# Optimization experiments

Measured on AMD Instinct MI355X. Metric: run time of the kernel, lower is better.

## Reference

```python
import jax, jax.numpy as jnp
import numpy as np
from jax import lax

CH = 16      # channel_n
HID = 128    # hidden_n
WDIM = 128   # w_dim


def _sobel_weight():
    sx = np.array([[-1, 0, 1], [-2, 0, 2], [-1, 0, 1]], dtype=np.float32).reshape(1, 1, 3, 3)
    sy = np.array([[-1, -2, -1], [0, 0, 0], [1, 2, 1]], dtype=np.float32).reshape(1, 1, 3, 3)
    sx = np.repeat(sx, CH, axis=0)  # [16,1,3,3]
    sy = np.repeat(sy, CH, axis=0)  # [16,1,3,3]
    return jnp.asarray(np.concatenate([sx, sy], axis=0))  # [32,1,3,3] torch grouped-conv OIHW layout


def setup_inputs() -> dict:
    key = jax.random.key(0)
    k1, k2, k3, k4 = jax.random.split(key, 4)
    B, H, W = 8, 96, 96
    x = jax.random.uniform(k1, (B, CH, H, W), dtype=jnp.float32)
    w = jax.random.normal(k2, (B, WDIM), dtype=jnp.float32)
    sobel = _sobel_weight()
    # update_net params. NOTE: original fills W2 with 0.0 (trivial delta); we use
    W1 = jax.random.normal(k3, (HID, 3 * CH + WDIM), dtype=jnp.float32) * 0.05
    b1 = jnp.zeros((HID,), dtype=jnp.float32)
    W2 = jax.random.normal(k4, (CH, HID), dtype=jnp.float32) * 0.02
    return {"x": x, "w": w, "sobel": sobel, "W1": W1, "b1": b1, "W2": W2, "steps": 64}


def _living_mask(alpha):
    # max_pool2d(3, stride=1, pad=1) > 0.1 ; torch pads with -inf for max pool
    m = lax.reduce_window(alpha, -jnp.inf, lax.max, (1, 1, 3, 3), (1, 1, 1, 1), 'SAME')
    return m > 0.1


def reference(x, w, sobel, W1, b1, W2, steps):
    B, _, H, Wd = x.shape
    w_exp = jnp.broadcast_to(w[:, :, None, None], (B, WDIM, H, Wd))

    def step(xc, key):
        pre_life = _living_mask(xc[:, 3:4])
        perception = lax.conv_general_dilated(
            xc, sobel, (1, 1), 'SAME', feature_group_count=CH,
            dimension_numbers=('NCHW', 'OIHW', 'NCHW'))  # [B,32,H,W]
        comb = jnp.concatenate([xc, perception, w_exp], axis=1)  # [B,176,H,W]
        h = jax.nn.relu(jnp.einsum('bchw,nc->bnhw', comb, W1) + b1[None, :, None, None])
        delta = jnp.einsum('bnhw,cn->bchw', h, W2)
        alpha = xc[:, 3:4]
        upd = (jax.random.uniform(key, alpha.shape) < 0.5) & (alpha > 0.1)
        xn = xc + delta * upd.astype(xc.dtype)
        life = pre_life & _living_mask(xn[:, 3:4])
        xn = xn * life.astype(xn.dtype)
        return xn, None

    keys = jax.random.split(jax.random.key(42), steps)
    x_final, _ = lax.scan(step, x, keys)
    return x_final
```

## Files before the change

### kernel.cpp

```cpp
#include <hip/hip_runtime.h>
#include <stdint.h>


#define CHN 16
#define HIDN 128
#define WD 128
#define NB 8
#define NH 96
#define NW 96
#define NSTEPS 64
#define TW 16
#define TH 4
#define PLANE (NH*NW)
#define TILES_X (NW/TW)
#define TILES_Y (NH/TH)
#define TPI (TILES_X*TILES_Y)
#define NBLK (NB*TPI)
#define HW_ (TH+2)
#define WW_ (TW+2)
#define NF4 (HW_*WW_*4)
#define NT 256

typedef float v2f __attribute__((ext_vector_type(2)));

__host__ __device__ __forceinline__ uint32_t rotl(uint32_t v, int d){ return (v<<d)|(v>>(32-d)); }

__host__ __device__ __forceinline__ void threefry2x32(uint32_t k0, uint32_t k1,
                                                      uint32_t x0, uint32_t x1,
                                                      uint32_t &o0, uint32_t &o1){
  uint32_t k2 = k0 ^ k1 ^ 0x1BD11BDAu;
  x0 += k0; x1 += k1;
  x0 += x1; x1 = rotl(x1,13); x1 ^= x0;
  x0 += x1; x1 = rotl(x1,15); x1 ^= x0;
  x0 += x1; x1 = rotl(x1,26); x1 ^= x0;
  x0 += x1; x1 = rotl(x1, 6); x1 ^= x0;
  x0 += k1; x1 += k2 + 1u;
  x0 += x1; x1 = rotl(x1,17); x1 ^= x0;
  x0 += x1; x1 = rotl(x1,29); x1 ^= x0;
  x0 += x1; x1 = rotl(x1,16); x1 ^= x0;
  x0 += x1; x1 = rotl(x1,24); x1 ^= x0;
  x0 += k2; x1 += k0 + 2u;
  x0 += x1; x1 = rotl(x1,13); x1 ^= x0;
  x0 += x1; x1 = rotl(x1,15); x1 ^= x0;
  x0 += x1; x1 = rotl(x1,26); x1 ^= x0;
  x0 += x1; x1 = rotl(x1, 6); x1 ^= x0;
  x0 += k0; x1 += k1 + 3u;
  x0 += x1; x1 = rotl(x1,17); x1 ^= x0;
  x0 += x1; x1 = rotl(x1,29); x1 ^= x0;
  x0 += x1; x1 = rotl(x1,16); x1 ^= x0;
  x0 += x1; x1 = rotl(x1,24); x1 ^= x0;
  x0 += k1; x1 += k2 + 4u;
  x0 += x1; x1 = rotl(x1,13); x1 ^= x0;
  x0 += x1; x1 = rotl(x1,15); x1 ^= x0;
  x0 += x1; x1 = rotl(x1,26); x1 ^= x0;
  x0 += x1; x1 = rotl(x1, 6); x1 ^= x0;
  x0 += k2; x1 += k0 + 5u;
  o0 = x0; o1 = x1;
}

__global__ __launch_bounds__(256) void nca_pre(
    const float* __restrict__ w, const float* __restrict__ W1,
    const float* __restrict__ b1, const float* __restrict__ W2,
    float* __restrict__ w1eff, float* __restrict__ w2t, float* __restrict__ c1)
{
  const int b = blockIdx.x, t = threadIdx.x;
  if (b == 0){
    for (int idx = t; idx < HIDN*32; idx += 256){
      int n = idx >> 5, k = idx & 31;
      float v;
      if (k < 16) v = W1[n*176 + k];
      else { int cc = k - 16; v = W1[n*176 + 16 + 2*cc] + W1[n*176 + 17 + 2*cc]; }
      w1eff[idx] = v;
    }
    for (int idx = t; idx < HIDN*CHN; idx += 256){
      int n = idx >> 4, cc = idx & 15;
      w2t[idx] = W2[cc*HIDN + n];
    }
  }
  if (t < HIDN){
    float s = b1[t];
    const float* wrow = W1 + t*176 + 48;
    const float* wb = w + b*WD;
    #pragma unroll 8
    for (int k = 0; k < WD; ++k) s = fmaf(wrow[k], wb[k], s);
    c1[b*HIDN + t] = s;
  }
}

template<bool FIRST>
__global__ __launch_bounds__(NT, 4) void nca_step(
    const float* __restrict__ Xin,
    const unsigned char* __restrict__ Mp,
    const float* __restrict__ w1eff, const float* __restrict__ w2t,
    const float* __restrict__ c1,
    uint32_t key0, uint32_t key1,
    float* __restrict__ Yn, unsigned char* __restrict__ Mn)
{
  __shared__ __align__(16) float w1s[64*32];
  __shared__ __align__(16) float xs[HW_][WW_][20];
  __shared__ float ya[TH+4][TW+4];
  __shared__ float lifes[HW_][WW_];
  __shared__ float ufs[64];

  float* red2p = &xs[0][0][0];
  #define RED2(bk,ch,p) red2p[((((bk)<<4)+(ch))<<6)+(p)]

  const int T = blockIdx.x;
  const int b = T & 7;
  const int t = T >> 3;
  const int tw0 = (t % TILES_X)*TW, th0 = (t / TILES_X)*TH;
  const int tid = threadIdx.x;

  {
    const float4* src = (const float4*)(w1eff + 64*32);
    float4* dst = (float4*)w1s;
    #pragma unroll
    for (int i = 0; i < 2; ++i) dst[tid + i*NT] = src[tid + i*NT];
  }

  if (FIRST){
    for (int idx = tid; idx < CHN*HW_*WW_; idx += NT){
      int ch = idx / (HW_*WW_), rem = idx % (HW_*WW_);
      int hh = rem / WW_, ww = rem % WW_;
      int g2 = th0 - 1 + hh, w2 = tw0 - 1 + ww;
      float v = 0.f;
      if ((unsigned)g2 < NH && (unsigned)w2 < NW)
        v = Xin[((b*CHN + ch)*NH + g2)*NW + w2];
      xs[hh][ww][ch] = v;
    }
  } else {
    if (tid < (TH+4)*(TW+4)){
      int hh = tid / (TW+4), ww = tid % (TW+4);
      int g2 = th0 - 2 + hh, w2 = tw0 - 2 + ww;
      float v = 0.f;
      if ((unsigned)g2 < NH && (unsigned)w2 < NW)
        v = Xin[(size_t)(b*PLANE + g2*NW + w2)*CHN + 3];
      ya[hh][ww] = v;
    }
    float4 xr[2];
    #pragma unroll
    for (int i = 0; i < 2; ++i){
      int idx = tid + i*NT;
      float4 v = make_float4(0.f,0.f,0.f,0.f);
      if (idx < NF4){
        int hh = idx / (WW_*4);
        int rem = idx % (WW_*4);
        int ww = rem >> 2, k4 = rem & 3;
        int g2 = th0 - 1 + hh, w2 = tw0 - 1 + ww;
        if ((unsigned)g2 < NH && (unsigned)w2 < NW)
          v = *(const float4*)(Xin + (size_t)(b*PLANE + g2*NW + w2)*CHN + k4*4);
      }
      xr[i] = v;
    }
    __syncthreads();
    if (tid < HW_*WW_){
      int hh = tid / WW_, ww = tid % WW_;
      int g2 = th0 - 1 + hh, w2 = tw0 - 1 + ww;
      float lf = 0.f;
      if ((unsigned)g2 < NH && (unsigned)w2 < NW){
        float mx = ya[hh][ww];
        #pragma unroll
        for (int dr = 0; dr < 3; ++dr)
          #pragma unroll
          for (int dc = 0; dc < 3; ++dc)
            mx = fmaxf(mx, ya[hh+dr][ww+dc]);
        lf = (Mp[b*PLANE + g2*NW + w2] && (mx > 0.1f)) ? 1.f : 0.f;
      }
      lifes[hh][ww] = lf;
    }
    __syncthreads();
    #pragma unroll
    for (int i = 0; i < 2; ++i){
      int idx = tid + i*NT;
      if (idx < NF4){
        int hh = idx / (WW_*4);
        int rem = idx % (WW_*4);
        int ww = rem >> 2, k4 = rem & 3;
        float lf = lifes[hh][ww];
        float4 v = xr[i];
        v.x *= lf; v.y *= lf; v.z *= lf; v.w *= lf;
        *(float4*)&xs[hh][ww][k4*4] = v;
      }
    }
  }
  __syncthreads();

  const int px = tid & 63;
  const int q  = tid >> 6;
  const int c = px & 15, r = px >> 4;
  const int gh = th0 + r, gw = tw0 + c;
  const int pos = b*PLANE + gh*NW + gw;

  #define LD4(dr,dc,k4) (*(const float4*)&xs[r+(dr)][c+(dc)][(k4)*4])
  const v2f two = (v2f){2.f, 2.f};
  float4 xc4[4];
  v2f xp[8], pp[8];
  #pragma unroll
  for (int k4 = 0; k4 < 4; ++k4){
    xc4[k4] = LD4(1,1,k4);
    xp[2*k4]   = (v2f){xc4[k4].x, xc4[k4].y};
    xp[2*k4+1] = (v2f){xc4[k4].z, xc4[k4].w};
  }
  #pragma unroll
  for (int k4 = 0; k4 < 2; ++k4){
    float4 a = LD4(0,2,k4), b0 = LD4(0,0,k4);
    float4 d = LD4(1,2,k4), e = LD4(1,0,k4);
    float4 f = LD4(2,2,k4), g = LD4(2,0,k4);
    v2f a0 = (v2f){a.x,a.y}, a1 = (v2f){a.z,a.w};
    v2f b0v= (v2f){b0.x,b0.y},b1v= (v2f){b0.z,b0.w};
    v2f d0 = (v2f){d.x,d.y}, d1 = (v2f){d.z,d.w};
    v2f e0 = (v2f){e.x,e.y}, e1 = (v2f){e.z,e.w};
    v2f f0 = (v2f){f.x,f.y}, f1 = (v2f){f.z,f.w};
    v2f g0 = (v2f){g.x,g.y}, g1 = (v2f){g.z,g.w};
    pp[2*k4]   = (a0-b0v) + two*(d0-e0) + (f0-g0);
    pp[2*k4+1] = (a1-b1v) + two*(d1-e1) + (f1-g1);
  }
  #pragma unroll
  for (int k4 = 2; k4 < 4; ++k4){
    float4 a = LD4(2,0,k4), b0 = LD4(0,0,k4);
    float4 d = LD4(2,1,k4), e = LD4(0,1,k4);
    float4 f = LD4(2,2,k4), g = LD4(0,2,k4);
    v2f a0 = (v2f){a.x,a.y}, a1 = (v2f){a.z,a.w};
    v2f b0v= (v2f){b0.x,b0.y},b1v= (v2f){b0.z,b0.w};
    v2f d0 = (v2f){d.x,d.y}, d1 = (v2f){d.z,d.w};
    v2f e0 = (v2f){e.x,e.y}, e1 = (v2f){e.z,e.w};
    v2f f0 = (v2f){f.x,f.y}, f1 = (v2f){f.z,f.w};
    v2f g0 = (v2f){g.x,g.y}, g1 = (v2f){g.z,g.w};
    pp[2*k4]   = (a0-b0v) + two*(d0-e0) + (f0-g0);
    pp[2*k4+1] = (a1-b1v) + two*(d1-e1) + (f1-g1);
  }
  #undef LD4

  if (q == 0){
    uint32_t o0, o1;
    threefry2x32(key0, key1, 0u, (uint32_t)pos, o0, o1);
    ufs[px] = ((((o0 ^ o1) >> 31) == 0u) && (xc4[0].w > 0.1f)) ? 1.f : 0.f;
  } else if (q == 1){
    float mx = xs[r][c][3];
    #pragma unroll
    for (int dr = 0; dr < 3; ++dr)
      #pragma unroll
      for (int dc = 0; dc < 3; ++dc)
        mx = fmaxf(mx, xs[r+dr][c+dc][3]);
    Mn[pos] = (mx > 0.1f) ? (unsigned char)1 : (unsigned char)0;
  }

  const int qq = __builtin_amdgcn_readfirstlane(q);
  float4 myx = xc4[0];
  if (qq == 1) myx = xc4[1];
  else if (qq == 2) myx = xc4[2];
  else if (qq == 3) myx = xc4[3];

  v2f acc2[8];
  #pragma unroll
  for (int i = 0; i < 8; ++i) acc2[i] = (v2f){0.f, 0.f};
  const int nbase = qq << 5;
  const float* c1b = c1 + b*HIDN;

  if (qq < 2){
    #pragma unroll 2
    for (int nn = 0; nn < 32; ++nn){
      const int n = nbase + nn;
      const v2f* wx = (const v2f*)(w1eff + (n << 5));
      v2f h01 = (v2f){c1b[n], 0.f};
      v2f h23 = (v2f){0.f, 0.f};
      #pragma unroll
      for (int k = 0; k < 8; ++k){
        h01 = __builtin_elementwise_fma(xp[k], wx[k],   h01);
        h23 = __builtin_elementwise_fma(pp[k], wx[8+k], h23);
      }
      float hv = fmaxf((h01.x + h01.y) + (h23.x + h23.y), 0.f);
      v2f hvv = (v2f){hv, hv};
      const v2f* w2p = (const v2f*)(w2t + (n << 4));
      #pragma unroll
      for (int cc2 = 0; cc2 < 8; ++cc2)
        acc2[cc2] = __builtin_elementwise_fma(hvv, w2p[cc2], acc2[cc2]);
    }
  } else {
    #pragma unroll 2
    for (int nn = 0; nn < 32; ++nn){
      const int n = nbase + nn;
      const v2f* wx = (const v2f*)(w1s + ((n - 64) << 5));
      v2f h01 = (v2f){c1b[n], 0.f};
      v2f h23 = (v2f){0.f, 0.f};
      #pragma unroll
      for (int k = 0; k < 8; ++k){
        h01 = __builtin_elementwise_fma(xp[k], wx[k],   h01);
        h23 = __builtin_elementwise_fma(pp[k], wx[8+k], h23);
      }
      float hv = fmaxf((h01.x + h01.y) + (h23.x + h23.y), 0.f);
      v2f hvv = (v2f){hv, hv};
      const v2f* w2p = (const v2f*)(w2t + (n << 4));
      #pragma unroll
      for (int cc2 = 0; cc2 < 8; ++cc2)
        acc2[cc2] = __builtin_elementwise_fma(hvv, w2p[cc2], acc2[cc2]);
    }
  }

  __syncthreads();

  if (q >= 2){
    #pragma unroll
    for (int cc2 = 0; cc2 < 8; ++cc2){
      RED2(q-2, 2*cc2  , px) = acc2[cc2].x;
      RED2(q-2, 2*cc2+1, px) = acc2[cc2].y;
    }
  }
  __syncthreads();
  if (q < 2){
    #pragma unroll
    for (int cc2 = 0; cc2 < 8; ++cc2){
      acc2[cc2].x += RED2(q, 2*cc2  , px);
      acc2[cc2].y += RED2(q, 2*cc2+1, px);
    }
    #pragma unroll
    for (int cc2 = 0; cc2 < 8; ++cc2){
      RED2(q, 2*cc2  , px) = acc2[cc2].x;
      RED2(q, 2*cc2+1, px) = acc2[cc2].y;
    }
  }
  __syncthreads();

  {
    float uf = ufs[px];
    int ch = q << 2;
    float v0 = RED2(0, ch+0, px) + RED2(1, ch+0, px);
    float v1 = RED2(0, ch+1, px) + RED2(1, ch+1, px);
    float v2 = RED2(0, ch+2, px) + RED2(1, ch+2, px);
    float v3 = RED2(0, ch+3, px) + RED2(1, ch+3, px);
    float4 o = make_float4(fmaf(v0, uf, myx.x), fmaf(v1, uf, myx.y),
                           fmaf(v2, uf, myx.z), fmaf(v3, uf, myx.w));
    *(float4*)(Yn + (size_t)pos*CHN + q*4) = o;
  }
  #undef RED2
}

__global__ __launch_bounds__(256) void nca_final(
    const float* __restrict__ Yp, const unsigned char* __restrict__ Mp,
    float* __restrict__ out)
{
  __shared__ float ya[TH+4][TW+4];
  __shared__ float lifes[TH][TW];
  const int T = blockIdx.x;
  const int b = T & 7;
  const int t = T >> 3;
  const int tw0 = (t % TILES_X)*TW, th0 = (t / TILES_X)*TH;
  const int tid = threadIdx.x;
  if (tid < (TH+4)*(TW+4)){
    int hh = tid / (TW+4), ww = tid % (TW+4);
    int g2 = th0 - 2 + hh, w2 = tw0 - 2 + ww;
    float v = 0.f;
    if ((unsigned)g2 < NH && (unsigned)w2 < NW)
      v = Yp[(size_t)(b*PLANE + g2*NW + w2)*CHN + 3];
    ya[hh][ww] = v;
  }
  __syncthreads();
  if (tid < TH*TW){
    int i = tid >> 4, j = tid & 15;
    float mx = ya[i+2][j+2];
    #pragma unroll
    for (int dr = 0; dr < 3; ++dr)
      #pragma unroll
      for (int dc = 0; dc < 3; ++dc)
        mx = fmaxf(mx, ya[i+1+dr][j+1+dc]);
    lifes[i][j] = (Mp[b*PLANE + (th0+i)*NW + (tw0+j)] && (mx > 0.1f)) ? 1.f : 0.f;
  }
  __syncthreads();
  for (int idx = tid; idx < CHN*TH*TW; idx += 256){
    int ch = idx >> 6, p = idx & 63;
    int i = p >> 4, j = p & 15;
    int pos = b*PLANE + (th0+i)*NW + (tw0+j);
    out[((b*CHN + ch)*NH + th0 + i)*NW + tw0 + j] = Yp[(size_t)pos*CHN + ch] * lifes[i][j];
  }
}

extern "C" void kernel_launch(void* const* d_in, const int* in_sizes, int n_in,
                              void* d_out, int out_size, void* d_ws, size_t ws_size,
                              hipStream_t stream) {
  const float* x  = (const float*)d_in[0];
  const float* w  = (const float*)d_in[1];
  const float* W1 = (const float*)d_in[3];
  const float* b1 = (const float*)d_in[4];
  const float* W2 = (const float*)d_in[5];
  float* out = (float*)d_out;
  char* ws = (char*)d_ws;

  size_t off = 0;
  float*    w1eff = (float*)(ws + off);    off += (size_t)HIDN*32*4;
  float*    w2t   = (float*)(ws + off);    off += (size_t)HIDN*CHN*4;
  float*    c1    = (float*)(ws + off);    off += (size_t)NB*HIDN*4;
  float*    Yb0   = (float*)(ws + off);    off += (size_t)NB*CHN*PLANE*4;
  float*    Yb1   = (float*)(ws + off);    off += (size_t)NB*CHN*PLANE*4;
  unsigned char* Mb0 = (unsigned char*)(ws + off); off += (size_t)NB*PLANE;
  unsigned char* Mb1 = (unsigned char*)(ws + off); off += (size_t)NB*PLANE;
  (void)ws_size; (void)in_sizes; (void)n_in; (void)out_size;

  uint32_t k0[NSTEPS], k1[NSTEPS];
  for (int s = 0; s < NSTEPS; ++s) threefry2x32(0u, 42u, 0u, (uint32_t)s, k0[s], k1[s]);

  nca_pre<<<dim3(NB), dim3(256), 0, stream>>>(w, W1, b1, W2, w1eff, w2t, c1);

  nca_step<true><<<dim3(NBLK), dim3(NT), 0, stream>>>(
      x, Mb1 , w1eff, w2t, c1, k0[0], k1[0], Yb0, Mb0);
  for (int s = 1; s < NSTEPS; ++s){
    const float* Yp = (s & 1) ? Yb0 : Yb1;
    float*       Yn = (s & 1) ? Yb1 : Yb0;
    const unsigned char* Mq = (s & 1) ? Mb0 : Mb1;
    unsigned char*       Mn = (s & 1) ? Mb1 : Mb0;
    nca_step<false><<<dim3(NBLK), dim3(NT), 0, stream>>>(
        Yp, Mq, w1eff, w2t, c1, k0[s], k1[s], Yn, Mn);
  }
  nca_final<<<dim3(NBLK), dim3(256), 0, stream>>>(Yb1, Mb1, out);
}
```

Before: 1.198 ms.

## Process two pixels per thread with taller step tiles to reuse weights

The step kernel tile grows from 16x4 to 16x8 pixels, and each thread now computes two pixel rows (A and B) that share every loaded W1/W2 weight value. This halves weight loads per FMA and halves the block count per step, cutting per-block overhead such as the shared-memory weight copy. The cost is higher register pressure (launch bounds reduced from 4 to 3 waves), fewer blocks (576 vs 1152) for the GPU's compute units, and a larger shared-memory footprint.

```diff
diff --git a/kernel.cpp b/kernel.cpp
--- a/kernel.cpp
+++ b/kernel.cpp
@@ -9,17 +9,27 @@
 #define NH 96
 #define NW 96
 #define NSTEPS 64
+#define PLANE (NH*NW)
+#define NT 256
+
 #define TW 16
 #define TH 4
-#define PLANE (NH*NW)
 #define TILES_X (NW/TW)
 #define TILES_Y (NH/TH)
 #define TPI (TILES_X*TILES_Y)
 #define NBLK (NB*TPI)
-#define HW_ (TH+2)
-#define WW_ (TW+2)
-#define NF4 (HW_*WW_*4)
-#define NT 256
+
+#define STW 16
+#define STH 8
+#define S_TILES_X (NW/STW)
+#define S_TILES_Y (NH/STH)
+#define S_TPI (S_TILES_X*S_TILES_Y)
+#define S_NBLK (NB*S_TPI)
+#define SHW (STH+2)
+#define SWW (STW+2)
+#define S_NF4 (SHW*SWW*4)
+#define XS_F (SHW*SWW*20)
+#define W1S_F (64*32)
 
 typedef float v2f __attribute__((ext_vector_type(2)));
 
@@ -87,114 +97,10 @@
   }
 }
 
-template<bool FIRST>
-__global__ __launch_bounds__(NT, 4) void nca_step(
-    const float* __restrict__ Xin,
-    const unsigned char* __restrict__ Mp,
-    const float* __restrict__ w1eff, const float* __restrict__ w2t,
-    const float* __restrict__ c1,
-    uint32_t key0, uint32_t key1,
-    float* __restrict__ Yn, unsigned char* __restrict__ Mn)
-{
-  __shared__ __align__(16) float w1s[64*32];
-  __shared__ __align__(16) float xs[HW_][WW_][20];
-  __shared__ float ya[TH+4][TW+4];
-  __shared__ float lifes[HW_][WW_];
-  __shared__ float ufs[64];
-
-  float* red2p = &xs[0][0][0];
-  #define RED2(bk,ch,p) red2p[((((bk)<<4)+(ch))<<6)+(p)]
-
-  const int T = blockIdx.x;
-  const int b = T & 7;
-  const int t = T >> 3;
-  const int tw0 = (t % TILES_X)*TW, th0 = (t / TILES_X)*TH;
-  const int tid = threadIdx.x;
-
-  {
-    const float4* src = (const float4*)(w1eff + 64*32);
-    float4* dst = (float4*)w1s;
-    #pragma unroll
-    for (int i = 0; i < 2; ++i) dst[tid + i*NT] = src[tid + i*NT];
-  }
-
-  if (FIRST){
-    for (int idx = tid; idx < CHN*HW_*WW_; idx += NT){
-      int ch = idx / (HW_*WW_), rem = idx % (HW_*WW_);
-      int hh = rem / WW_, ww = rem % WW_;
-      int g2 = th0 - 1 + hh, w2 = tw0 - 1 + ww;
-      float v = 0.f;
-      if ((unsigned)g2 < NH && (unsigned)w2 < NW)
-        v = Xin[((b*CHN + ch)*NH + g2)*NW + w2];
-      xs[hh][ww][ch] = v;
-    }
-  } else {
-    if (tid < (TH+4)*(TW+4)){
-      int hh = tid / (TW+4), ww = tid % (TW+4);
-      int g2 = th0 - 2 + hh, w2 = tw0 - 2 + ww;
-      float v = 0.f;
-      if ((unsigned)g2 < NH && (unsigned)w2 < NW)
-        v = Xin[(size_t)(b*PLANE + g2*NW + w2)*CHN + 3];
-      ya[hh][ww] = v;
-    }
-    float4 xr[2];
-    #pragma unroll
-    for (int i = 0; i < 2; ++i){
-      int idx = tid + i*NT;
-      float4 v = make_float4(0.f,0.f,0.f,0.f);
-      if (idx < NF4){
-        int hh = idx / (WW_*4);
-        int rem = idx % (WW_*4);
-        int ww = rem >> 2, k4 = rem & 3;
-        int g2 = th0 - 1 + hh, w2 = tw0 - 1 + ww;
-        if ((unsigned)g2 < NH && (unsigned)w2 < NW)
-          v = *(const float4*)(Xin + (size_t)(b*PLANE + g2*NW + w2)*CHN + k4*4);
-      }
-      xr[i] = v;
-    }
-    __syncthreads();
-    if (tid < HW_*WW_){
-      int hh = tid / WW_, ww = tid % WW_;
-      int g2 = th0 - 1 + hh, w2 = tw0 - 1 + ww;
-      float lf = 0.f;
-      if ((unsigned)g2 < NH && (unsigned)w2 < NW){
-        float mx = ya[hh][ww];
-        #pragma unroll
-        for (int dr = 0; dr < 3; ++dr)
-          #pragma unroll
-          for (int dc = 0; dc < 3; ++dc)
-            mx = fmaxf(mx, ya[hh+dr][ww+dc]);
-        lf = (Mp[b*PLANE + g2*NW + w2] && (mx > 0.1f)) ? 1.f : 0.f;
-      }
-      lifes[hh][ww] = lf;
-    }
-    __syncthreads();
-    #pragma unroll
-    for (int i = 0; i < 2; ++i){
-      int idx = tid + i*NT;
-      if (idx < NF4){
-        int hh = idx / (WW_*4);
-        int rem = idx % (WW_*4);
-        int ww = rem >> 2, k4 = rem & 3;
-        float lf = lifes[hh][ww];
-        float4 v = xr[i];
-        v.x *= lf; v.y *= lf; v.z *= lf; v.w *= lf;
-        *(float4*)&xs[hh][ww][k4*4] = v;
-      }
-    }
-  }
-  __syncthreads();
-
-  const int px = tid & 63;
-  const int q  = tid >> 6;
-  const int c = px & 15, r = px >> 4;
-  const int gh = th0 + r, gw = tw0 + c;
-  const int pos = b*PLANE + gh*NW + gw;
-
-  #define LD4(dr,dc,k4) (*(const float4*)&xs[r+(dr)][c+(dc)][(k4)*4])
+__device__ __forceinline__ void perceive(const float* smp, int r, int c,
+                                         float4* xc4, v2f* xp, v2f* pp){
   const v2f two = (v2f){2.f, 2.f};
-  float4 xc4[4];
-  v2f xp[8], pp[8];
+  #define LD4(dr,dc,k4) (*(const float4*)(smp + ((r+(dr))*SWW + (c+(dc)))*20 + (k4)*4))
   #pragma unroll
   for (int k4 = 0; k4 < 4; ++k4){
     xc4[k4] = LD4(1,1,k4);
@@ -230,30 +136,147 @@
     pp[2*k4+1] = (a1-b1v) + two*(d1-e1) + (f1-g1);
   }
   #undef LD4
+}
+
+template<bool FIRST>
+__global__ __launch_bounds__(NT, 3) void nca_step(
+    const float* __restrict__ Xin,
+    const unsigned char* __restrict__ Mp,
+    const float* __restrict__ w1eff, const float* __restrict__ w2t,
+    const float* __restrict__ c1,
+    uint32_t key0, uint32_t key1,
+    float* __restrict__ Yn, unsigned char* __restrict__ Mn)
+{
+  __shared__ __align__(16) float sm[XS_F + W1S_F];
+  __shared__ float ya[STH+4][STW+4];
+  __shared__ float lifes[SHW][SWW];
+  __shared__ float ufs[128];
+
+  float* w1s = sm + XS_F;
+  #define RED2(bk,ch,p) sm[(((bk)*16+(ch))*128)+(p)]
+
+  const int T = blockIdx.x;
+  const int b = T & 7;
+  const int t = T >> 3;
+  const int tw0 = (t % S_TILES_X)*STW, th0 = (t / S_TILES_X)*STH;
+  const int tid = threadIdx.x;
+
+  {
+    const float4* src = (const float4*)(w1eff + 64*32);
+    float4* dst = (float4*)w1s;
+    dst[tid]      = src[tid];
+    dst[tid + NT] = src[tid + NT];
+  }
+
+  if (FIRST){
+    for (int idx = tid; idx < CHN*SHW*SWW; idx += NT){
+      int ch = idx / (SHW*SWW), rem = idx % (SHW*SWW);
+      int hh = rem / SWW, ww = rem % SWW;
+      int g2 = th0 - 1 + hh, w2 = tw0 - 1 + ww;
+      float v = 0.f;
+      if ((unsigned)g2 < NH && (unsigned)w2 < NW)
+        v = Xin[((b*CHN + ch)*NH + g2)*NW + w2];
+      sm[(hh*SWW + ww)*20 + ch] = v;
+    }
+  } else {
+    if (tid < (STH+4)*(STW+4)){
+      int hh = tid / (STW+4), ww = tid % (STW+4);
+      int g2 = th0 - 2 + hh, w2 = tw0 - 2 + ww;
+      float v = 0.f;
+      if ((unsigned)g2 < NH && (unsigned)w2 < NW)
+        v = Xin[(size_t)(b*PLANE + g2*NW + w2)*CHN + 3];
+      ya[hh][ww] = v;
+    }
+    float4 xr[3];
+    #pragma unroll
+    for (int i = 0; i < 3; ++i){
+      int idx = tid + i*NT;
+      float4 v = make_float4(0.f,0.f,0.f,0.f);
+      if (idx < S_NF4){
+        int hh = idx / (SWW*4);
+        int rem = idx % (SWW*4);
+        int ww = rem >> 2, k4 = rem & 3;
+        int g2 = th0 - 1 + hh, w2 = tw0 - 1 + ww;
+        if ((unsigned)g2 < NH && (unsigned)w2 < NW)
+          v = *(const float4*)(Xin + (size_t)(b*PLANE + g2*NW + w2)*CHN + k4*4);
+      }
+      xr[i] = v;
+    }
+    __syncthreads();
+    if (tid < SHW*SWW){
+      int hh = tid / SWW, ww = tid % SWW;
+      int g2 = th0 - 1 + hh, w2 = tw0 - 1 + ww;
+      float lf = 0.f;
+      if ((unsigned)g2 < NH && (unsigned)w2 < NW){
+        float mx = ya[hh][ww];
+        #pragma unroll
+        for (int dr = 0; dr < 3; ++dr)
+          #pragma unroll
+          for (int dc = 0; dc < 3; ++dc)
+            mx = fmaxf(mx, ya[hh+dr][ww+dc]);
+        lf = (Mp[b*PLANE + g2*NW + w2] && (mx > 0.1f)) ? 1.f : 0.f;
+      }
+      lifes[hh][ww] = lf;
+    }
+    __syncthreads();
+    #pragma unroll
+    for (int i = 0; i < 3; ++i){
+      int idx = tid + i*NT;
+      if (idx < S_NF4){
+        int hh = idx / (SWW*4);
+        int rem = idx % (SWW*4);
+        int ww = rem >> 2, k4 = rem & 3;
+        float lf = lifes[hh][ww];
+        float4 v = xr[i];
+        v.x *= lf; v.y *= lf; v.z *= lf; v.w *= lf;
+        *(float4*)(sm + (hh*SWW + ww)*20 + k4*4) = v;
+      }
+    }
+  }
+  __syncthreads();
+
+  const int px = tid & 63;
+  const int q  = tid >> 6;
+  const int c = px & 15, rA = px >> 4;
+  const int rB = rA + 4;
+  const int gw = tw0 + c;
+  const int posA = b*PLANE + (th0 + rA)*NW + gw;
+  const int posB = posA + 4*NW;
+
+  float4 xcA[4], xcB[4];
+  v2f xpa[8], ppa[8], xpb[8], ppb[8];
+  perceive(sm, rA, c, xcA, xpa, ppa);
+  perceive(sm, rB, c, xcB, xpb, ppb);
 
   if (q == 0){
     uint32_t o0, o1;
-    threefry2x32(key0, key1, 0u, (uint32_t)pos, o0, o1);
-    ufs[px] = ((((o0 ^ o1) >> 31) == 0u) && (xc4[0].w > 0.1f)) ? 1.f : 0.f;
+    threefry2x32(key0, key1, 0u, (uint32_t)posA, o0, o1);
+    ufs[px]    = ((((o0 ^ o1) >> 31) == 0u) && (xcA[0].w > 0.1f)) ? 1.f : 0.f;
+    threefry2x32(key0, key1, 0u, (uint32_t)posB, o0, o1);
+    ufs[px+64] = ((((o0 ^ o1) >> 31) == 0u) && (xcB[0].w > 0.1f)) ? 1.f : 0.f;
   } else if (q == 1){
-    float mx = xs[r][c][3];
+    float mxA = sm[(rA*SWW + c)*20 + 3];
+    float mxB = sm[(rB*SWW + c)*20 + 3];
     #pragma unroll
     for (int dr = 0; dr < 3; ++dr)
       #pragma unroll
-      for (int dc = 0; dc < 3; ++dc)
-        mx = fmaxf(mx, xs[r+dr][c+dc][3]);
-    Mn[pos] = (mx > 0.1f) ? (unsigned char)1 : (unsigned char)0;
+      for (int dc = 0; dc < 3; ++dc){
+        mxA = fmaxf(mxA, sm[((rA+dr)*SWW + (c+dc))*20 + 3]);
+        mxB = fmaxf(mxB, sm[((rB+dr)*SWW + (c+dc))*20 + 3]);
+      }
+    Mn[posA] = (mxA > 0.1f) ? (unsigned char)1 : (unsigned char)0;
+    Mn[posB] = (mxB > 0.1f) ? (unsigned char)1 : (unsigned char)0;
   }
 
   const int qq = __builtin_amdgcn_readfirstlane(q);
-  float4 myx = xc4[0];
-  if (qq == 1) myx = xc4[1];
-  else if (qq == 2) myx = xc4[2];
-  else if (qq == 3) myx = xc4[3];
-
-  v2f acc2[8];
+  float4 myxA = xcA[0], myxB = xcB[0];
+  if (qq == 1){ myxA = xcA[1]; myxB = xcB[1]; }
+  else if (qq == 2){ myxA = xcA[2]; myxB = xcB[2]; }
+  else if (qq == 3){ myxA = xcA[3]; myxB = xcB[3]; }
+
+  v2f acA[8], acB[8];
   #pragma unroll
-  for (int i = 0; i < 8; ++i) acc2[i] = (v2f){0.f, 0.f};
+  for (int i = 0; i < 8; ++i){ acA[i] = (v2f){0.f,0.f}; acB[i] = (v2f){0.f,0.f}; }
   const int nbase = qq << 5;
   const float* c1b = c1 + b*HIDN;
 
@@ -262,38 +285,52 @@
     for (int nn = 0; nn < 32; ++nn){
       const int n = nbase + nn;
       const v2f* wx = (const v2f*)(w1eff + (n << 5));
-      v2f h01 = (v2f){c1b[n], 0.f};
-      v2f h23 = (v2f){0.f, 0.f};
+      v2f hA01 = (v2f){c1b[n], 0.f}, hA23 = (v2f){0.f, 0.f};
+      v2f hB01 = (v2f){c1b[n], 0.f}, hB23 = (v2f){0.f, 0.f};
       #pragma unroll
       for (int k = 0; k < 8; ++k){
-        h01 = __builtin_elementwise_fma(xp[k], wx[k],   h01);
-        h23 = __builtin_elementwise_fma(pp[k], wx[8+k], h23);
-      }
-      float hv = fmaxf((h01.x + h01.y) + (h23.x + h23.y), 0.f);
-      v2f hvv = (v2f){hv, hv};
+        v2f w0 = wx[k], w1v = wx[8+k];
+        hA01 = __builtin_elementwise_fma(xpa[k], w0,  hA01);
+        hA23 = __builtin_elementwise_fma(ppa[k], w1v, hA23);
+        hB01 = __builtin_elementwise_fma(xpb[k], w0,  hB01);
+        hB23 = __builtin_elementwise_fma(ppb[k], w1v, hB23);
+      }
+      float hvA = fmaxf((hA01.x + hA01.y) + (hA23.x + hA23.y), 0.f);
+      float hvB = fmaxf((hB01.x + hB01.y) + (hB23.x + hB23.y), 0.f);
+      v2f hA = (v2f){hvA, hvA}, hB = (v2f){hvB, hvB};
       const v2f* w2p = (const v2f*)(w2t + (n << 4));
       #pragma unroll
-      for (int cc2 = 0; cc2 < 8; ++cc2)
-        acc2[cc2] = __builtin_elementwise_fma(hvv, w2p[cc2], acc2[cc2]);
+      for (int cc2 = 0; cc2 < 8; ++cc2){
+        v2f wv = w2p[cc2];
+        acA[cc2] = __builtin_elementwise_fma(hA, wv, acA[cc2]);
+        acB[cc2] = __builtin_elementwise_fma(hB, wv, acB[cc2]);
+      }
     }
   } else {
-    #pragma unroll 2
+    #pragma unroll 1
     for (int nn = 0; nn < 32; ++nn){
       const int n = nbase + nn;
       const v2f* wx = (const v2f*)(w1s + ((n - 64) << 5));
-      v2f h01 = (v2f){c1b[n], 0.f};
-      v2f h23 = (v2f){0.f, 0.f};
+      v2f hA01 = (v2f){c1b[n], 0.f}, hA23 = (v2f){0.f, 0.f};
+      v2f hB01 = (v2f){c1b[n], 0.f}, hB23 = (v2f){0.f, 0.f};
       #pragma unroll
       for (int k = 0; k < 8; ++k){
-        h01 = __builtin_elementwise_fma(xp[k], wx[k],   h01);
-        h23 = __builtin_elementwise_fma(pp[k], wx[8+k], h23);
-      }
-      float hv = fmaxf((h01.x + h01.y) + (h23.x + h23.y), 0.f);
-      v2f hvv = (v2f){hv, hv};
+        v2f w0 = wx[k], w1v = wx[8+k];
+        hA01 = __builtin_elementwise_fma(xpa[k], w0,  hA01);
+        hA23 = __builtin_elementwise_fma(ppa[k], w1v, hA23);
+        hB01 = __builtin_elementwise_fma(xpb[k], w0,  hB01);
+        hB23 = __builtin_elementwise_fma(ppb[k], w1v, hB23);
+      }
+      float hvA = fmaxf((hA01.x + hA01.y) + (hA23.x + hA23.y), 0.f);
+      float hvB = fmaxf((hB01.x + hB01.y) + (hB23.x + hB23.y), 0.f);
+      v2f hA = (v2f){hvA, hvA}, hB = (v2f){hvB, hvB};
       const v2f* w2p = (const v2f*)(w2t + (n << 4));
       #pragma unroll
-      for (int cc2 = 0; cc2 < 8; ++cc2)
-        acc2[cc2] = __builtin_elementwise_fma(hvv, w2p[cc2], acc2[cc2]);
+      for (int cc2 = 0; cc2 < 8; ++cc2){
+        v2f wv = w2p[cc2];
+        acA[cc2] = __builtin_elementwise_fma(hA, wv, acA[cc2]);
+        acB[cc2] = __builtin_elementwise_fma(hB, wv, acB[cc2]);
+      }
     }
   }
 
@@ -302,35 +339,48 @@
   if (q >= 2){
     #pragma unroll
     for (int cc2 = 0; cc2 < 8; ++cc2){
-      RED2(q-2, 2*cc2  , px) = acc2[cc2].x;
-      RED2(q-2, 2*cc2+1, px) = acc2[cc2].y;
+      RED2(q-2, 2*cc2  , px)    = acA[cc2].x;
+      RED2(q-2, 2*cc2+1, px)    = acA[cc2].y;
+      RED2(q-2, 2*cc2  , px+64) = acB[cc2].x;
+      RED2(q-2, 2*cc2+1, px+64) = acB[cc2].y;
     }
   }
   __syncthreads();
   if (q < 2){
     #pragma unroll
     for (int cc2 = 0; cc2 < 8; ++cc2){
-      acc2[cc2].x += RED2(q, 2*cc2  , px);
-      acc2[cc2].y += RED2(q, 2*cc2+1, px);
+      acA[cc2].x += RED2(q, 2*cc2  , px);
+      acA[cc2].y += RED2(q, 2*cc2+1, px);
+      acB[cc2].x += RED2(q, 2*cc2  , px+64);
+      acB[cc2].y += RED2(q, 2*cc2+1, px+64);
     }
     #pragma unroll
     for (int cc2 = 0; cc2 < 8; ++cc2){
-      RED2(q, 2*cc2  , px) = acc2[cc2].x;
-      RED2(q, 2*cc2+1, px) = acc2[cc2].y;
+      RED2(q, 2*cc2  , px)    = acA[cc2].x;
+      RED2(q, 2*cc2+1, px)    = acA[cc2].y;
+      RED2(q, 2*cc2  , px+64) = acB[cc2].x;
+      RED2(q, 2*cc2+1, px+64) = acB[cc2].y;
     }
   }
   __syncthreads();
 
   {
-    float uf = ufs[px];
+    float ufA = ufs[px], ufB = ufs[px+64];
     int ch = q << 2;
-    float v0 = RED2(0, ch+0, px) + RED2(1, ch+0, px);
-    float v1 = RED2(0, ch+1, px) + RED2(1, ch+1, px);
-    float v2 = RED2(0, ch+2, px) + RED2(1, ch+2, px);
-    float v3 = RED2(0, ch+3, px) + RED2(1, ch+3, px);
-    float4 o = make_float4(fmaf(v0, uf, myx.x), fmaf(v1, uf, myx.y),
-                           fmaf(v2, uf, myx.z), fmaf(v3, uf, myx.w));
-    *(float4*)(Yn + (size_t)pos*CHN + q*4) = o;
+    float a0 = RED2(0, ch+0, px) + RED2(1, ch+0, px);
+    float a1 = RED2(0, ch+1, px) + RED2(1, ch+1, px);
+    float a2 = RED2(0, ch+2, px) + RED2(1, ch+2, px);
+    float a3 = RED2(0, ch+3, px) + RED2(1, ch+3, px);
+    float4 oA = make_float4(fmaf(a0, ufA, myxA.x), fmaf(a1, ufA, myxA.y),
+                            fmaf(a2, ufA, myxA.z), fmaf(a3, ufA, myxA.w));
+    *(float4*)(Yn + (size_t)posA*CHN + q*4) = oA;
+    float b0 = RED2(0, ch+0, px+64) + RED2(1, ch+0, px+64);
+    float b1v = RED2(0, ch+1, px+64) + RED2(1, ch+1, px+64);
+    float b2 = RED2(0, ch+2, px+64) + RED2(1, ch+2, px+64);
+    float b3 = RED2(0, ch+3, px+64) + RED2(1, ch+3, px+64);
+    float4 oB = make_float4(fmaf(b0, ufB, myxB.x), fmaf(b1v, ufB, myxB.y),
+                            fmaf(b2, ufB, myxB.z), fmaf(b3, ufB, myxB.w));
+    *(float4*)(Yn + (size_t)posB*CHN + q*4) = oB;
   }
   #undef RED2
 }
@@ -400,14 +450,14 @@
 
   nca_pre<<<dim3(NB), dim3(256), 0, stream>>>(w, W1, b1, W2, w1eff, w2t, c1);
 
-  nca_step<true><<<dim3(NBLK), dim3(NT), 0, stream>>>(
+  nca_step<true><<<dim3(S_NBLK), dim3(NT), 0, stream>>>(
       x, Mb1 , w1eff, w2t, c1, k0[0], k1[0], Yb0, Mb0);
   for (int s = 1; s < NSTEPS; ++s){
     const float* Yp = (s & 1) ? Yb0 : Yb1;
     float*       Yn = (s & 1) ? Yb1 : Yb0;
     const unsigned char* Mq = (s & 1) ? Mb0 : Mb1;
     unsigned char*       Mn = (s & 1) ? Mb1 : Mb0;
-    nca_step<false><<<dim3(NBLK), dim3(NT), 0, stream>>>(
+    nca_step<false><<<dim3(S_NBLK), dim3(NT), 0, stream>>>(
         Yp, Mq, w1eff, w2t, c1, k0[s], k1[s], Yn, Mn);
   }
   nca_final<<<dim3(NBLK), dim3(256), 0, stream>>>(Yb1, Mb1, out);
```

Measured after the change: 2.230 ms. +86.1%, slower.
